# Kernel tuning notes

Measured on AMD Instinct MI355X. Metric: run time of the kernel, lower is better.

The kernel has to match this reference:

```python
import jax, jax.numpy as jnp
import numpy as np

NHEADS = 4   # attention heads (search_cfg.nheads)
WS = 7       # spatial search window side -> WS*WS candidates per query
PS = 3       # patch size for distance computation (search_cfg.ps)
K = 16       # top-k neighbors kept (search_cfg.k)


def layer_norm_2d(vid, w, b, eps=1e-6):
    # LayerNorm over channel dim at every (t,h,w) location; vid (B,T,C,H,W)
    mu = vid.mean(axis=2, keepdims=True)
    var = vid.var(axis=2, keepdims=True)
    y = (vid - mu) / jnp.sqrt(var + eps)
    return y * w[None, None, :, None, None] + b[None, None, :, None, None]


def conv1x1(vid, w, b):
    # 1x1 ConvQKV projection: vid (B,T,C,H,W), w (O,C)
    return jnp.einsum('btchw,oc->btohw', vid, w) + b[None, None, :, None, None]


def box_sum(x, ps):
    # sum over centered ps x ps patch (zero pad); x (..., H, W)
    r = ps // 2
    H, W = x.shape[-2], x.shape[-1]
    xp = jnp.pad(x, [(0, 0)] * (x.ndim - 2) + [(r, r), (r, r)])
    out = jnp.zeros_like(x)
    ah, aw = x.ndim - 2, x.ndim - 1
    for dy in range(ps):
        for dx in range(ps):
            s = jax.lax.dynamic_slice_in_dim(xp, dy, H, ah)
            s = jax.lax.dynamic_slice_in_dim(s, dx, W, aw)
            out = out + s
    return out


def nl_search(q, k):
    # patch-based non-local search: q,k (B,T,HD,c,H,W)
    B, T, HD, c, H, W = q.shape
    r = WS // 2
    kp = jnp.pad(k, ((0, 0),) * 4 + ((r, r), (r, r)))  # zero pad = invalid candidates score ~0
    offs = jnp.stack(jnp.meshgrid(jnp.arange(WS), jnp.arange(WS), indexing='ij'), -1).reshape(-1, 2)

    @jax.checkpoint
    def step(carry, off):
        dy, dx = off[0], off[1]
        ksh = jax.lax.dynamic_slice(kp, (0, 0, 0, 0, dy, dx), (B, T, HD, c, H, W))
        s = (q * ksh).sum(axis=3)      # pixel inner products (B,T,HD,H,W)
        s = box_sum(s, PS)             # patch inner products
        return carry, s

    _, scores = jax.lax.scan(step, 0, offs)        # (WS*WS,B,T,HD,H,W)
    scores = jnp.moveaxis(scores, 0, -1)           # (B,T,HD,H,W,WS*WS)
    dists, inds = jax.lax.top_k(scores, K)         # top-k neighbors per query
    return dists, inds


def nl_stack(v, weights, inds):
    # gather the K selected neighbor values, weighted; v (B,T,HD,c,H,W)
    B, T, HD, c, H, W = v.shape
    r = WS // 2
    vp = jnp.pad(v, ((0, 0),) * 4 + ((r, r), (r, r)))
    Hp, Wp = H + 2 * r, W + 2 * r
    row = jnp.arange(H)[:, None, None] + inds // WS   # (B,T,HD,H,W,K)
    col = jnp.arange(W)[None, :, None] + inds % WS
    lin = (row * Wp + col).reshape(B, T, HD, 1, H * W * K)
    vf = vp.reshape(B, T, HD, c, Hp * Wp)
    g = jnp.take_along_axis(vf, jnp.broadcast_to(lin, (B, T, HD, c, H * W * K)), axis=-1)
    g = g.reshape(B, T, HD, c, H, W, K)
    g = g * weights[:, :, :, None]                    # weight each neighbor
    # -> (B*T, HD*c, K, H, W) stack for Conv3d projection
    return jnp.transpose(g, (0, 1, 2, 3, 6, 4, 5)).reshape(B * T, HD * c, K, H, W)


def proj3d(stack, w, b):
    # Conv3d(io_dim, io_dim, (K,3,3), stride=(K,1,1), pad=(0,1,1), groups=NHEADS)
    out = jax.lax.conv_general_dilated(
        stack, w, window_strides=(K, 1, 1),
        padding=((0, 0), (1, 1), (1, 1)),
        dimension_numbers=('NCDHW', 'OIDHW', 'NCDHW'),
        feature_group_count=NHEADS)
    return out[:, :, 0] + b[None, :, None, None]


def setup_inputs() -> dict:
    key = jax.random.key(0)
    ks = jax.random.split(key, 8)
    B, T, C, H, W = 1, 4, 128, 96, 96
    sc = 1.0 / np.sqrt(C)
    inp = {
        'vid': jax.random.normal(ks[0], (B, T, C, H, W), jnp.float32),
        'ln_w': jnp.ones((C,), jnp.float32),
        'ln_b': jnp.zeros((C,), jnp.float32),
        'wq': jax.random.normal(ks[1], (C, C), jnp.float32) * sc,
        'bq': jnp.zeros((C,), jnp.float32),
        'wk': jax.random.normal(ks[2], (C, C), jnp.float32) * sc,
        'bk': jnp.zeros((C,), jnp.float32),
        'wv': jax.random.normal(ks[3], (C, C), jnp.float32) * sc,
        'bv': jnp.zeros((C,), jnp.float32),
        'proj_w': jax.random.normal(ks[4], (C, C // NHEADS, K, 3, 3), jnp.float32) * 0.02,
        'proj_b': jnp.zeros((C,), jnp.float32),
    }
    return inp


def reference(vid, ln_w, ln_b, wq, bq, wk, bk, wv, bv, proj_w, proj_b):
    B, T, C, H, W = vid.shape
    x = layer_norm_2d(vid, ln_w, ln_b)
    q = conv1x1(x, wq, bq)
    k = conv1x1(x, wk, bk)
    v = conv1x1(x, wv, bv)
    hd = lambda t: t.reshape(B, T, NHEADS, C // NHEADS, H, W)
    q, k, v = hd(q), hd(k), hd(v)
    dists, inds = nl_search(q, k)                 # k-NN search
    weights = jax.nn.softmax(dists, axis=-1)      # normalize over K
    stack = nl_stack(v, weights, inds)            # neighbor stacking
    out = proj3d(stack, proj_w, proj_b)           # conv projection collapses K
    return out.reshape(B, T, C, H, W)
```

## Files before the change

kernel.cpp:

```cpp
#include <hip/hip_runtime.h>


typedef float  f32x4  __attribute__((ext_vector_type(4)));
typedef __bf16 bf16x8 __attribute__((ext_vector_type(8)));
typedef __bf16 bf16x4 __attribute__((ext_vector_type(4)));

__global__ __launch_bounds__(256) void prep_kernel(
    const float* __restrict__ wq, const float* __restrict__ wk, const float* __restrict__ wv,
    const float* __restrict__ pw, float* __restrict__ Wt, __bf16* __restrict__ pwt) {
  int idx = blockIdx.x * 256 + threadIdx.x;
  const int NPW = 4 * 16 * 9 * 32 * 32;
  if (idx < NPW) {
    int i  = idx & 31;
    int ol = (idx >> 5) & 31;
    int d  = (idx >> 10) % 9;
    int r  = (idx >> 10) / 9;
    int kd = r & 15;
    int g  = r >> 4;
    int o  = g * 32 + ol;
    pwt[idx] = (__bf16)pw[((o * 32 + i) * 16 + kd) * 9 + d];
  } else {
    int widx = idx - NPW;
    if (widx < 128 * 384) {
      int o = widx % 384;
      int c = widx / 384;
      const float* __restrict__ src = (o < 128) ? wq : (o < 256 ? wk : wv);
      Wt[widx] = src[(o & 127) * 128 + c];
    }
  }
}

__global__ __launch_bounds__(64) void ln_stats_kernel(
    const float* __restrict__ vid, float* __restrict__ mu, float* __restrict__ rs) {
  int pix = blockIdx.x * 64 + threadIdx.x;
  int f = blockIdx.y;
  const float* __restrict__ vp = vid + (size_t)f * 128 * 9216 + pix;
  float s = 0.f, s2 = 0.f;
  #pragma unroll 8
  for (int c = 0; c < 128; ++c) { float x = vp[(size_t)c * 9216]; s += x; s2 += x * x; }
  float m_ = s * (1.f / 128.f);
  float v_ = fmaxf(s2 * (1.f / 128.f) - m_ * m_, 0.f);
  mu[f * 9216 + pix] = m_;
  rs[f * 9216 + pix] = rsqrtf(v_ + 1e-6f);
}

__global__ __launch_bounds__(512) void qkv_gemm_kernel(
    const float* __restrict__ vid, const float* __restrict__ mu, const float* __restrict__ rs,
    const float* __restrict__ lnw, const float* __restrict__ lnb,
    const float* __restrict__ Wt, const float* __restrict__ bq, const float* __restrict__ bk,
    const float* __restrict__ bv, float* __restrict__ qb, float* __restrict__ kb,
    __bf16* __restrict__ vbbf) {
  __shared__ __align__(16) float Xs[32][128];
  __shared__ __align__(16) float Ws[32][128];
  __shared__ float muL[128], rsL[128], lwS[128], lbS[128];
  int tid = threadIdx.x;
  int mt = blockIdx.y;
  int N0 = blockIdx.x * 128;
  int f  = mt / 72;
  int pf = (mt % 72) * 128;

  if (tid < 128) {
    muL[tid] = mu[f * 9216 + pf + tid];
    rsL[tid] = rs[f * 9216 + pf + tid];
  } else if (tid < 256) {
    int t2 = tid - 128;
    lwS[t2] = lnw[t2];
    lbS[t2] = lnb[t2];
  }

  int tx = tid & 15, ty = tid >> 4;
  int m0 = ty * 4;
  int sm = tid & 127;
  int sk = tid >> 7;
  float acc[4][8];
  #pragma unroll
  for (int a = 0; a < 4; ++a)
    #pragma unroll
    for (int b = 0; b < 8; ++b) acc[a][b] = 0.f;

  const size_t vbase = (size_t)f * 128 * 9216 + pf;
  float xr[8], wr[8];

  #pragma unroll
  for (int it = 0; it < 8; ++it) {
    int kk = sk + 4 * it;
    xr[it] = vid[vbase + (size_t)kk * 9216 + sm];
    wr[it] = Wt[(size_t)kk * 384 + N0 + sm];
  }
  __syncthreads();
  #pragma unroll
  for (int it = 0; it < 8; ++it) {
    int kk = sk + 4 * it;
    Xs[kk][sm] = (xr[it] - muL[sm]) * rsL[sm] * lwS[kk] + lbS[kk];
    Ws[kk][sm] = wr[it];
  }
  __syncthreads();

  for (int kc = 0; kc < 4; ++kc) {
    if (kc < 3) {
      #pragma unroll
      for (int it = 0; it < 8; ++it) {
        int kk = sk + 4 * it;
        int c = (kc + 1) * 32 + kk;
        xr[it] = vid[vbase + (size_t)c * 9216 + sm];
        wr[it] = Wt[(size_t)c * 384 + N0 + sm];
      }
    }
    #pragma unroll 4
    for (int kk = 0; kk < 32; ++kk) {
      float xa[4], wa[8];
      *(float4*)&xa[0] = *(const float4*)&Xs[kk][m0];
      *(float4*)&wa[0] = *(const float4*)&Ws[kk][tx * 4];
      *(float4*)&wa[4] = *(const float4*)&Ws[kk][64 + tx * 4];
      #pragma unroll
      for (int a = 0; a < 4; ++a)
        #pragma unroll
        for (int b = 0; b < 8; ++b)
          acc[a][b] = fmaf(xa[a], wa[b], acc[a][b]);
    }
    if (kc < 3) {
      __syncthreads();
      #pragma unroll
      for (int it = 0; it < 8; ++it) {
        int kk = sk + 4 * it;
        int c = (kc + 1) * 32 + kk;
        Xs[kk][sm] = (xr[it] - muL[sm]) * rsL[sm] * lwS[c] + lbS[c];
        Ws[kk][sm] = wr[it];
      }
      __syncthreads();
    }
  }

  int sel = blockIdx.x;
  int nlo = tx * 4, nhi = 64 + tx * 4;
  int hlo = nlo >> 5, clo = nlo & 31;
  int hhi = nhi >> 5, chi = nhi & 31;
  const float* __restrict__ bias = (sel == 0) ? bq : (sel == 1 ? bk : bv);
  float4 blo = make_float4(bias[nlo], bias[nlo + 1], bias[nlo + 2], bias[nlo + 3]);
  float4 bhi = make_float4(bias[nhi], bias[nhi + 1], bias[nhi + 2], bias[nhi + 3]);
  size_t base_lo = (size_t)(f * 4 + hlo) * 9216 * 32 + clo;
  size_t base_hi = (size_t)(f * 4 + hhi) * 9216 * 32 + chi;
  if (sel < 2) {
    float* __restrict__ dst = (sel == 0) ? qb : kb;
    #pragma unroll
    for (int a = 0; a < 4; ++a) {
      size_t poff = (size_t)(pf + m0 + a) * 32;
      *(float4*)&dst[base_lo + poff] = make_float4(acc[a][0] + blo.x, acc[a][1] + blo.y,
                                                   acc[a][2] + blo.z, acc[a][3] + blo.w);
      *(float4*)&dst[base_hi + poff] = make_float4(acc[a][4] + bhi.x, acc[a][5] + bhi.y,
                                                   acc[a][6] + bhi.z, acc[a][7] + bhi.w);
    }
  } else {
    #pragma unroll
    for (int a = 0; a < 4; ++a) {
      size_t poff = (size_t)(pf + m0 + a) * 32;
      bf16x4 lo4, hi4;
      lo4[0] = (__bf16)(acc[a][0] + blo.x); lo4[1] = (__bf16)(acc[a][1] + blo.y);
      lo4[2] = (__bf16)(acc[a][2] + blo.z); lo4[3] = (__bf16)(acc[a][3] + blo.w);
      hi4[0] = (__bf16)(acc[a][4] + bhi.x); hi4[1] = (__bf16)(acc[a][5] + bhi.y);
      hi4[2] = (__bf16)(acc[a][6] + bhi.z); hi4[3] = (__bf16)(acc[a][7] + bhi.w);
      *(bf16x4*)&vbbf[base_lo + poff] = lo4;
      *(bf16x4*)&vbbf[base_hi + poff] = hi4;
    }
  }
}

__global__ __launch_bounds__(256) void search_kernel(
    const float* __restrict__ qb, const float* __restrict__ kb,
    float* __restrict__ wgtb, int* __restrict__ indb) {
  __shared__ __align__(16) float klds[400 * 32];
  __shared__ float slds[2][200];
  int tid = threadIdx.x;
  int th = blockIdx.y;
  int tile = blockIdx.x;
  int ty0 = (tile >> 3) * 12, tx0 = (tile & 7) * 12;
  const float* __restrict__ kbase = kb + (size_t)th * 9216 * 32;

  for (int i = tid; i < 400 * 8; i += 256) {
    int pix = i >> 3, c4 = i & 7;
    int ry = pix / 20, rx = pix % 20;
    int gy = ty0 - 4 + ry, gx = tx0 - 4 + rx;
    float4 val = make_float4(0.f, 0.f, 0.f, 0.f);
    if ((unsigned)gy < 96u && (unsigned)gx < 96u)
      val = *(const float4*)&kbase[(size_t)(gy * 96 + gx) * 32 + c4 * 4];
    *(float4*)&klds[pix * 32 + ((c4 ^ (pix & 7)) << 2)] = val;
  }

  int sy = tid / 14, sx = tid % 14;
  bool active = tid < 196;
  int gy = ty0 - 1 + sy, gx = tx0 - 1 + sx;
  bool qok = active && (unsigned)gy < 96u && (unsigned)gx < 96u;
  float4 qv[8];
  #pragma unroll
  for (int j = 0; j < 8; ++j) qv[j] = make_float4(0.f, 0.f, 0.f, 0.f);
  if (qok) {
    const float* __restrict__ qp = qb + ((size_t)th * 9216 + gy * 96 + gx) * 32;
    #pragma unroll
    for (int j = 0; j < 8; ++j) qv[j] = *(const float4*)&qp[j * 4];
  }
  bool inner = active && sy >= 1 && sy <= 12 && sx >= 1 && sx <= 12;
  int py = ty0 + sy - 1, px = tx0 + sx - 1;

  float tv[16]; int tix[16];
  #pragma unroll
  for (int j = 0; j < 16; ++j) { tv[j] = -3.0e38f; tix[j] = 0; }
  __syncthreads();

  for (int oi = 0; oi < 49; ++oi) {
    int dy = oi / 7, dx = oi % 7;
    if (active) {
      int p = (sy + dy) * 20 + (sx + dx);
      const float* __restrict__ kp = &klds[p * 32];
      int sw = p & 7;
      float sdot = 0.f;
      #pragma unroll
      for (int j = 0; j < 8; ++j) {
        float4 kv = *(const float4*)&kp[(j ^ sw) << 2];
        sdot += qv[j].x * kv.x + qv[j].y * kv.y + qv[j].z * kv.z + qv[j].w * kv.w;
      }
      slds[oi & 1][tid] = sdot;
    }
    __syncthreads();
    if (inner) {
      const float* __restrict__ sb = slds[oi & 1];
      float sc = 0.f;
      #pragma unroll
      for (int a = 0; a < 3; ++a)
        #pragma unroll
        for (int b = 0; b < 3; ++b)
          sc += sb[(sy - 1 + a) * 14 + (sx - 1 + b)];
      float cv = sc; int ci = oi; bool ins = false;
      #pragma unroll
      for (int j = 0; j < 16; ++j) {
        bool sw2 = ins || (cv > tv[j]);
        float pv = tv[j]; int pi = tix[j];
        tv[j]  = sw2 ? cv : pv;
        tix[j] = sw2 ? ci : pi;
        cv = sw2 ? pv : cv;
        ci = sw2 ? pi : ci;
        ins = sw2;
      }
    }
  }

  if (inner) {
    float mx = tv[0];
    float e[16], ssum = 0.f;
    #pragma unroll
    for (int j = 0; j < 16; ++j) { e[j] = __expf(tv[j] - mx); ssum += e[j]; }
    float inv = 1.f / ssum;
    size_t base = ((size_t)th * 9216 + py * 96 + px) * 16;
    #pragma unroll
    for (int j = 0; j < 4; ++j) {
      *(float4*)&wgtb[base + j * 4] =
          make_float4(e[j*4] * inv, e[j*4+1] * inv, e[j*4+2] * inv, e[j*4+3] * inv);
      *(int4*)&indb[base + j * 4] = make_int4(tix[j*4], tix[j*4+1], tix[j*4+2], tix[j*4+3]);
    }
  }
}

__global__ __launch_bounds__(512) void proj_kernel(
    const __bf16* __restrict__ vb, const float* __restrict__ wgtb, const int* __restrict__ indb,
    const __bf16* __restrict__ pwt, const float* __restrict__ pb, float* __restrict__ outp) {
  __shared__ __align__(16) __bf16 Alds[324 * 40];
  __shared__ __align__(16) __bf16 Blds[288 * 40];
  int tid = threadIdx.x;
  int bid = blockIdx.x;
  int wg = (bid & 7) * 72 + (bid >> 3);
  int th = wg / 36;
  int tile = wg % 36;
  int g = th & 3;
  int ty0 = (tile / 6) * 16, tx0 = (tile % 6) * 16;
  int lane = tid & 63, wid = tid >> 6;
  int kg = lane >> 4, lr = lane & 15;

  bool gact = tid < 324;
  int ry = tid / 18, rx = tid % 18;
  int gy = ty0 - 1 + ry, gx = tx0 - 1 + rx;
  bool inb = gact && (unsigned)gy < 96u && (unsigned)gx < 96u;
  const __bf16* __restrict__ vbase = vb + (size_t)th * 9216 * 32;
  size_t pxoff = inb ? (size_t)(gy * 96 + gx) : 0;
  const int*   __restrict__ ibase = indb + ((size_t)th * 9216 + pxoff) * 16;
  const float* __restrict__ wbase = wgtb + ((size_t)th * 9216 + pxoff) * 16;

  f32x4 acc[2][2];
  acc[0][0] = (f32x4)(0.0f); acc[0][1] = (f32x4)(0.0f);
  acc[1][0] = (f32x4)(0.0f); acc[1][1] = (f32x4)(0.0f);

  int4 iw_i = make_int4(0, 0, 0, 0);
  float4 iw_w = make_float4(0.f, 0.f, 0.f, 0.f);
  int4 vr[4];
  vr[0] = vr[1] = vr[2] = vr[3] = make_int4(0, 0, 0, 0);
  float wcur = 0.f;

  if (inb) {
    iw_i = *(const int4*)&ibase[0];
    iw_w = *(const float4*)&wbase[0];
    int ind0 = iw_i.x;
    int ny = gy + ind0 / 7 - 3, nx = gx + ind0 % 7 - 3;
    if ((unsigned)ny < 96u && (unsigned)nx < 96u) {
      const int4* __restrict__ vp = (const int4*)(vbase + (size_t)(ny * 96 + nx) * 32);
      vr[0] = vp[0]; vr[1] = vp[1]; vr[2] = vp[2]; vr[3] = vp[3];
    }
    wcur = iw_w.x;
  }

  for (int kdb = 0; kdb < 4; ++kdb) {
    #pragma unroll
    for (int kb = 0; kb < 4; ++kb) {
      int kd = kdb * 4 + kb;
      __syncthreads();
      if (gact) {
        __bf16 tmp[32];
        #pragma unroll
        for (int wv = 0; wv < 4; ++wv) {
          unsigned uu[4] = {(unsigned)vr[wv].x, (unsigned)vr[wv].y,
                            (unsigned)vr[wv].z, (unsigned)vr[wv].w};
          #pragma unroll
          for (int j2 = 0; j2 < 4; ++j2) {
            float lo = __uint_as_float(uu[j2] << 16);
            float hi = __uint_as_float(uu[j2] & 0xffff0000u);
            tmp[wv * 8 + j2 * 2]     = (__bf16)(lo * wcur);
            tmp[wv * 8 + j2 * 2 + 1] = (__bf16)(hi * wcur);
          }
        }
        __bf16* dst = &Alds[tid * 40];
        *(int4*)&dst[0]  = *(const int4*)&tmp[0];
        *(int4*)&dst[8]  = *(const int4*)&tmp[8];
        *(int4*)&dst[16] = *(const int4*)&tmp[16];
        *(int4*)&dst[24] = *(const int4*)&tmp[24];
      }
      {
        const __bf16* __restrict__ bsrc = pwt + (size_t)(g * 16 + kd) * 9216;
        #pragma unroll
        for (int itb = 0; itb < 3; ++itb) {
          int i = itb * 512 + tid;
          if (i < 1152) {
            int row = i >> 2, c = i & 3;
            *(int4*)&Blds[row * 40 + c * 8] = *(const int4*)&bsrc[row * 32 + c * 8];
          }
        }
      }
      __syncthreads();
      if (kd < 15) {
        int indn; float wn;
        if (kb == 3) {
          if (inb) {
            iw_i = *(const int4*)&ibase[kd + 1];
            iw_w = *(const float4*)&wbase[kd + 1];
          }
          indn = iw_i.x; wn = iw_w.x;
        } else {
          indn = (kb == 0) ? iw_i.y : (kb == 1) ? iw_i.z : iw_i.w;
          wn   = (kb == 0) ? iw_w.y : (kb == 1) ? iw_w.z : iw_w.w;
        }
        vr[0] = vr[1] = vr[2] = vr[3] = make_int4(0, 0, 0, 0);
        if (inb) {
          int ny = gy + indn / 7 - 3, nx = gx + indn % 7 - 3;
          if ((unsigned)ny < 96u && (unsigned)nx < 96u) {
            const int4* __restrict__ vp = (const int4*)(vbase + (size_t)(ny * 96 + nx) * 32);
            vr[0] = vp[0]; vr[1] = vp[1]; vr[2] = vp[2]; vr[3] = vp[3];
          }
        }
        wcur = wn;
      }
      #pragma unroll
      for (int d = 0; d < 9; ++d) {
        int dy = d / 3 - 1, dx = d % 3 - 1;
        bf16x8 b0 = *(const bf16x8*)&Blds[(d * 32 + lr) * 40 + kg * 8];
        bf16x8 b1 = *(const bf16x8*)&Blds[(d * 32 + 16 + lr) * 40 + kg * 8];
        #pragma unroll
        for (int mt = 0; mt < 2; ++mt) {
          int ryy = wid * 2 + mt + 1 + dy;
          int rxx = lr + 1 + dx;
          bf16x8 af = *(const bf16x8*)&Alds[(ryy * 18 + rxx) * 40 + kg * 8];
          acc[mt][0] = __builtin_amdgcn_mfma_f32_16x16x32_bf16(af, b0, acc[mt][0], 0, 0, 0);
          acc[mt][1] = __builtin_amdgcn_mfma_f32_16x16x32_bf16(af, b1, acc[mt][1], 0, 0, 0);
        }
      }
    }
  }

  int x0 = tx0 + kg * 4;
  int f = th >> 2;
  #pragma unroll
  for (int mt = 0; mt < 2; ++mt) {
    int y = ty0 + wid * 2 + mt;
    #pragma unroll
    for (int nt = 0; nt < 2; ++nt) {
      int o = g * 32 + nt * 16 + lr;
      float bias = pb[o];
      float4 res = make_float4(acc[mt][nt][0] + bias, acc[mt][nt][1] + bias,
                               acc[mt][nt][2] + bias, acc[mt][nt][3] + bias);
      *(float4*)&outp[(size_t)(f * 128 + o) * 9216 + y * 96 + x0] = res;
    }
  }
}

extern "C" void kernel_launch(void* const* d_in, const int* in_sizes, int n_in,
                              void* d_out, int out_size, void* d_ws, size_t ws_size,
                              hipStream_t stream) {
  const float* vid = (const float*)d_in[0];
  const float* lnw = (const float*)d_in[1];
  const float* lnb = (const float*)d_in[2];
  const float* wq  = (const float*)d_in[3];
  const float* bq  = (const float*)d_in[4];
  const float* wk  = (const float*)d_in[5];
  const float* bk  = (const float*)d_in[6];
  const float* wv_ = (const float*)d_in[7];
  const float* bv  = (const float*)d_in[8];
  const float* pw  = (const float*)d_in[9];
  const float* pb  = (const float*)d_in[10];
  float* outp = (float*)d_out;

  const size_t SZ_T  = (size_t)16 * 9216 * 32 * 4;
  const size_t SZ_TB = (size_t)16 * 9216 * 32 * 2;
  const size_t SZ_W  = (size_t)16 * 9216 * 16 * 4;
  const size_t SZ_WT = 128 * 384 * 4;
  const size_t SZ_PW = (size_t)4 * 16 * 9 * 32 * 32 * 2;
  const size_t SZ_MU = (size_t)4 * 9216 * 4;

  char* p = (char*)d_ws;
  float* qb = (float*)p;        p += SZ_T;
  float* kb = (float*)p;        p += SZ_T;
  __bf16* vbbf = (__bf16*)p;    p += SZ_TB;
  float* wgtb = (float*)p;      p += SZ_W;
  int*   indb = (int*)p;        p += SZ_W;
  float* Wt = (float*)p;        p += SZ_WT;
  __bf16* pwt = (__bf16*)p;     p += SZ_PW;
  float* mu = (float*)p;        p += SZ_MU;
  float* rs = (float*)p;

  prep_kernel<<<2496, 256, 0, stream>>>(wq, wk, wv_, pw, Wt, pwt);
  ln_stats_kernel<<<dim3(144, 4), 64, 0, stream>>>(vid, mu, rs);
  qkv_gemm_kernel<<<dim3(3, 288), 512, 0, stream>>>(vid, mu, rs, lnw, lnb, Wt, bq, bk, bv,
                                                    qb, kb, vbbf);
  search_kernel<<<dim3(64, 16), 256, 0, stream>>>(qb, kb, wgtb, indb);
  proj_kernel<<<576, 512, 0, stream>>>(vbbf, wgtb, indb, pwt, pb, outp);
}
```

Baseline: 238.6 us.

## Restructure NL search with 16x16 tiles, rolling K window, DPP box-sum, min/max top-k

The search kernel now uses 16x16 thread tiles, each producing 14x14 query outputs. The K halo is kept in a rolling 16-row LDS ring buffer that loads one new row per dy step instead of the whole 20x20 window, which shrinks LDS use and allows 3 blocks per CU. The horizontal part of the 3x3 box sum is done with DPP lane shifts and the vertical part via LDS at ±16. The top-k insertion is rewritten with fmax/fmin, and there is an extra barrier per dy to refill the ring.

```diff
diff --git a/kernel.cpp b/kernel.cpp
--- a/kernel.cpp
+++ b/kernel.cpp
@@ -4,6 +4,13 @@
 typedef float  f32x4  __attribute__((ext_vector_type(4)));
 typedef __bf16 bf16x8 __attribute__((ext_vector_type(8)));
 typedef __bf16 bf16x4 __attribute__((ext_vector_type(4)));
+
+__device__ __forceinline__ float dpp_shr1(float x) {
+  return __int_as_float(__builtin_amdgcn_update_dpp(0, __float_as_int(x), 0x111, 0xf, 0xf, false));
+}
+__device__ __forceinline__ float dpp_shl1(float x) {
+  return __int_as_float(__builtin_amdgcn_update_dpp(0, __float_as_int(x), 0x101, 0xf, 0xf, false));
+}
 
 __global__ __launch_bounds__(256) void prep_kernel(
     const float* __restrict__ wq, const float* __restrict__ wk, const float* __restrict__ wv,
@@ -165,80 +172,91 @@
   }
 }
 
-__global__ __launch_bounds__(256) void search_kernel(
+__global__ __launch_bounds__(256, 3) void search_kernel(
     const float* __restrict__ qb, const float* __restrict__ kb,
     float* __restrict__ wgtb, int* __restrict__ indb) {
-  __shared__ __align__(16) float klds[400 * 32];
-  __shared__ float slds[2][200];
+  __shared__ __align__(16) float klds[16 * 22 * 32];
+  __shared__ float slds[2][256];
   int tid = threadIdx.x;
   int th = blockIdx.y;
   int tile = blockIdx.x;
-  int ty0 = (tile >> 3) * 12, tx0 = (tile & 7) * 12;
+  int iy0 = (tile / 7) * 14, ix0 = (tile % 7) * 14;
   const float* __restrict__ kbase = kb + (size_t)th * 9216 * 32;
 
-  for (int i = tid; i < 400 * 8; i += 256) {
-    int pix = i >> 3, c4 = i & 7;
-    int ry = pix / 20, rx = pix % 20;
-    int gy = ty0 - 4 + ry, gx = tx0 - 4 + rx;
+  #pragma unroll
+  for (int it = 0; it < 11; ++it) {
+    int i = it * 256 + tid;
+    int r = i / 176, rem = i % 176;
+    int col = rem >> 3, c4 = rem & 7;
+    int gy = iy0 - 4 + r, gx = ix0 - 4 + col;
     float4 val = make_float4(0.f, 0.f, 0.f, 0.f);
     if ((unsigned)gy < 96u && (unsigned)gx < 96u)
       val = *(const float4*)&kbase[(size_t)(gy * 96 + gx) * 32 + c4 * 4];
-    *(float4*)&klds[pix * 32 + ((c4 ^ (pix & 7)) << 2)] = val;
-  }
-
-  int sy = tid / 14, sx = tid % 14;
-  bool active = tid < 196;
-  int gy = ty0 - 1 + sy, gx = tx0 - 1 + sx;
-  bool qok = active && (unsigned)gy < 96u && (unsigned)gx < 96u;
+    int p = r * 22 + col;
+    *(float4*)&klds[p * 32 + ((c4 ^ (p & 7)) << 2)] = val;
+  }
+
+  int sy = tid >> 4, sx = tid & 15;
+  int qy = iy0 - 1 + sy, qx = ix0 - 1 + sx;
+  bool qok = (unsigned)qy < 96u && (unsigned)qx < 96u;
   float4 qv[8];
   #pragma unroll
   for (int j = 0; j < 8; ++j) qv[j] = make_float4(0.f, 0.f, 0.f, 0.f);
   if (qok) {
-    const float* __restrict__ qp = qb + ((size_t)th * 9216 + gy * 96 + gx) * 32;
+    const float* __restrict__ qp = qb + ((size_t)th * 9216 + qy * 96 + qx) * 32;
     #pragma unroll
     for (int j = 0; j < 8; ++j) qv[j] = *(const float4*)&qp[j * 4];
   }
-  bool inner = active && sy >= 1 && sy <= 12 && sx >= 1 && sx <= 12;
-  int py = ty0 + sy - 1, px = tx0 + sx - 1;
+  bool inner = (sy >= 1) && (sy <= 14) && (sx >= 1) && (sx <= 14) && qok;
 
   float tv[16]; int tix[16];
   #pragma unroll
   for (int j = 0; j < 16; ++j) { tv[j] = -3.0e38f; tix[j] = 0; }
   __syncthreads();
 
-  for (int oi = 0; oi < 49; ++oi) {
-    int dy = oi / 7, dx = oi % 7;
-    if (active) {
-      int p = (sy + dy) * 20 + (sx + dx);
+  #pragma unroll 1
+  for (int dy = 0; dy < 7; ++dy) {
+    if (dy > 0) {
+      if (tid < 176) {
+        int col = tid >> 3, c4 = tid & 7;
+        int r = dy + 15;
+        int gy = iy0 - 4 + r, gx = ix0 - 4 + col;
+        float4 val = make_float4(0.f, 0.f, 0.f, 0.f);
+        if ((unsigned)gy < 96u && (unsigned)gx < 96u)
+          val = *(const float4*)&kbase[(size_t)(gy * 96 + gx) * 32 + c4 * 4];
+        int p = (r & 15) * 22 + col;
+        *(float4*)&klds[p * 32 + ((c4 ^ (p & 7)) << 2)] = val;
+      }
+      __syncthreads();
+    }
+    #pragma unroll 1
+    for (int dx = 0; dx < 7; ++dx) {
+      int oi = dy * 7 + dx;
+      int p = ((sy + dy) & 15) * 22 + (sx + dx);
       const float* __restrict__ kp = &klds[p * 32];
       int sw = p & 7;
       float sdot = 0.f;
       #pragma unroll
       for (int j = 0; j < 8; ++j) {
-        float4 kv = *(const float4*)&kp[(j ^ sw) << 2];
-        sdot += qv[j].x * kv.x + qv[j].y * kv.y + qv[j].z * kv.z + qv[j].w * kv.w;
-      }
-      slds[oi & 1][tid] = sdot;
-    }
-    __syncthreads();
-    if (inner) {
-      const float* __restrict__ sb = slds[oi & 1];
-      float sc = 0.f;
-      #pragma unroll
-      for (int a = 0; a < 3; ++a)
+        float4 kq = *(const float4*)&kp[(j ^ sw) << 2];
+        sdot += qv[j].x * kq.x + qv[j].y * kq.y + qv[j].z * kq.z + qv[j].w * kq.w;
+      }
+      float h = sdot + dpp_shr1(sdot) + dpp_shl1(sdot);
+      slds[oi & 1][tid] = h;
+      __syncthreads();
+      if (inner) {
+        const float* __restrict__ sb = slds[oi & 1];
+        float sc = h + sb[tid - 16] + sb[tid + 16];
+        float cv = sc; int ci = oi;
         #pragma unroll
-        for (int b = 0; b < 3; ++b)
-          sc += sb[(sy - 1 + a) * 14 + (sx - 1 + b)];
-      float cv = sc; int ci = oi; bool ins = false;
-      #pragma unroll
-      for (int j = 0; j < 16; ++j) {
-        bool sw2 = ins || (cv > tv[j]);
-        float pv = tv[j]; int pi = tix[j];
-        tv[j]  = sw2 ? cv : pv;
-        tix[j] = sw2 ? ci : pi;
-        cv = sw2 ? pv : cv;
-        ci = sw2 ? pi : ci;
-        ins = sw2;
+        for (int j = 0; j < 16; ++j) {
+          bool gt = cv > tv[j];
+          float mx = fmaxf(tv[j], cv);
+          float mn = fminf(tv[j], cv);
+          int nt = gt ? ci : tix[j];
+          ci = gt ? tix[j] : ci;
+          tv[j] = mx; cv = mn; tix[j] = nt;
+        }
       }
     }
   }
@@ -249,7 +267,7 @@
     #pragma unroll
     for (int j = 0; j < 16; ++j) { e[j] = __expf(tv[j] - mx); ssum += e[j]; }
     float inv = 1.f / ssum;
-    size_t base = ((size_t)th * 9216 + py * 96 + px) * 16;
+    size_t base = ((size_t)th * 9216 + qy * 96 + qx) * 16;
     #pragma unroll
     for (int j = 0; j < 4; ++j) {
       *(float4*)&wgtb[base + j * 4] =
@@ -435,6 +453,6 @@
   ln_stats_kernel<<<dim3(144, 4), 64, 0, stream>>>(vid, mu, rs);
   qkv_gemm_kernel<<<dim3(3, 288), 512, 0, stream>>>(vid, mu, rs, lnw, lnb, Wt, bq, bk, bv,
                                                     qb, kb, vbbf);
-  search_kernel<<<dim3(64, 16), 256, 0, stream>>>(qb, kb, wgtb, indb);
+  search_kernel<<<dim3(49, 16), 256, 0, stream>>>(qb, kb, wgtb, indb);
   proj_kernel<<<576, 512, 0, stream>>>(vbbf, wgtb, indb, pwt, pb, outp);
 }
```

Measured after the change: 229.5 us. -3.8%, faster.
